# Optimization experiments

Hardware: AMD Instinct MI355X
Metric: run time of the kernel (lower is better)

## Reference

```python
import jax, jax.numpy as jnp
import numpy as np

USER = 100000
ITEM = 200000
N = USER + ITEM
LATDIM = 64
N_LAYERS = 3
N_EDGES = 9600000


def setup_inputs() -> dict:
    key = jax.random.key(0)
    k1, k2, k3, k4, k5 = jax.random.split(key, 5)
    # xavier_uniform for [N, latdim]: bound = sqrt(6/(fan_in+fan_out))
    bu = float(np.sqrt(6.0 / (USER + LATDIM)))
    bi = float(np.sqrt(6.0 / (ITEM + LATDIM)))
    uEmbeds = jax.random.uniform(k1, (USER, LATDIM), jnp.float32, -bu, bu)
    iEmbeds = jax.random.uniform(k2, (ITEM, LATDIM), jnp.float32, -bi, bi)
    edge_row = jax.random.randint(k3, (N_EDGES,), 0, N, dtype=jnp.int32)
    edge_col = jax.random.randint(k4, (N_EDGES,), 0, N, dtype=jnp.int32)
    edge_val = jax.random.uniform(k5, (N_EDGES,), jnp.float32) * 0.01
    return {"uEmbeds": uEmbeds, "iEmbeds": iEmbeds,
            "edge_row": edge_row, "edge_col": edge_col, "edge_val": edge_val}


def _spmm(row, col, val, x):
    # sparse adj (COO) @ dense x: gather cols, scale, scatter-add to rows
    msgs = x[col] * val[:, None]                 # [E, D]
    return jax.ops.segment_sum(msgs, row, num_segments=N)  # [N, D]


def reference(uEmbeds, iEmbeds, edge_row, edge_col, edge_val):
    # forward_gcn: multi-layer propagation, sum of all layer embeddings
    embeds = jnp.concatenate([uEmbeds, iEmbeds], axis=0)  # [N, D]
    acc = embeds
    cur = embeds
    for _ in range(N_LAYERS):
        cur = _spmm(edge_row, edge_col, edge_val, cur)
        acc = acc + cur
    return acc[:USER], acc[USER:]
```

## Files before the change

### kernel.cpp

```cpp
#include <hip/hip_runtime.h>
#include <hip/hip_bf16.h>

#define USER_N   100000
#define ITEM_N   200000
#define N_NODES  300000
#define LATDIM   64
#define N_EDGES  9600000
#define N_LAYERS 3

#define CSHIFT   11
#define CROWS    2048
#define NCOARSE  ((N_NODES + CROWS - 1) / CROWS)
#define CHUNK    4096
#define NCHUNKS  ((N_EDGES + CHUNK - 1) / CHUNK)
#define GPA      512

__device__ __forceinline__ unsigned short f2bf(float f) {
    unsigned int u = __float_as_uint(f);
    u += 0x7FFFu + ((u >> 16) & 1u);
    return (unsigned short)(u >> 16);
}
__device__ __forceinline__ float bf2f(unsigned short h) {
    return __uint_as_float(((unsigned int)h) << 16);
}

__global__ void cvt_concat_kernel(const float* __restrict__ u,
                                  const float* __restrict__ it,
                                  ushort4* __restrict__ cur0,
                                  int n4u, int n4total) {
    int stride = gridDim.x * blockDim.x;
    for (int i = blockIdx.x * blockDim.x + threadIdx.x; i < n4total; i += stride) {
        float4 v = (i < n4u) ? ((const float4*)u)[i]
                             : ((const float4*)it)[i - n4u];
        ushort4 o;
        o.x = f2bf(v.x); o.y = f2bf(v.y); o.z = f2bf(v.z); o.w = f2bf(v.w);
        cur0[i] = o;
    }
}

__global__ void h1_kernel(const int* __restrict__ row, int* __restrict__ ccnt) {
    __shared__ int h[NCOARSE];
    int t = threadIdx.x;
    if (t < NCOARSE) h[t] = 0;
    __syncthreads();
    int stride = gridDim.x * blockDim.x;
    for (int e = blockIdx.x * blockDim.x + t; e < N_EDGES; e += stride)
        atomicAdd(&h[row[e] >> CSHIFT], 1);
    __syncthreads();
    if (t < NCOARSE && h[t]) atomicAdd(&ccnt[t], h[t]);
}

__global__ void scan_coarse_kernel(const int* __restrict__ ccnt,
                                   int* __restrict__ cbase,
                                   int* __restrict__ cursorA,
                                   int* __restrict__ rowPtr) {
    __shared__ int lds[256];
    int t = threadIdx.x;
    int v = (t < NCOARSE) ? ccnt[t] : 0;
    lds[t] = v;
    __syncthreads();
    for (int off = 1; off < 256; off <<= 1) {
        int add = (t >= off) ? lds[t - off] : 0;
        __syncthreads();
        lds[t] += add;
        __syncthreads();
    }
    if (t < NCOARSE) { int ex = lds[t] - v; cbase[t] = ex; cursorA[t] = ex; }
    if (t == NCOARSE - 1) cbase[NCOARSE] = lds[t];
    if (t == 0) rowPtr[N_NODES] = N_EDGES;
}

__global__ __launch_bounds__(256)
void passA_kernel(const int*   __restrict__ row,
                  const int*   __restrict__ col,
                  const float* __restrict__ val,
                  int*         __restrict__ cursorA,
                  int2*        __restrict__ tempA) {
    __shared__ int2 stage[CHUNK];
    __shared__ unsigned char cb[CHUNK];
    __shared__ int h[NCOARSE];
    __shared__ int cur[NCOARSE];
    int t = threadIdx.x;
    for (int cid = blockIdx.x; cid < NCHUNKS; cid += gridDim.x) {
        if (t < NCOARSE) h[t] = 0;
        __syncthreads();
        int e0 = cid * CHUNK;
        int e1 = e0 + CHUNK; if (e1 > N_EDGES) e1 = N_EDGES;
        for (int e = e0 + t; e < e1; e += 256) {
            int r = row[e];
            int c = r >> CSHIFT;
            stage[e - e0] = make_int2(((r & (CROWS - 1)) << 19) | col[e],
                                      __float_as_int(val[e]));
            cb[e - e0] = (unsigned char)c;
            atomicAdd(&h[c], 1);
        }
        __syncthreads();
        if (t < NCOARSE) {
            int n = h[t];
            cur[t] = n ? atomicAdd(&cursorA[t], n) : 0;
        }
        __syncthreads();
        for (int e = e0 + t; e < e1; e += 256) {
            int c = cb[e - e0];
            int pos = atomicAdd(&cur[c], 1);
            tempA[pos] = stage[e - e0];
        }
        __syncthreads();
    }
}

__global__ __launch_bounds__(1024)
void passB_kernel(const int*  __restrict__ cbase,
                  const int2* __restrict__ tempA,
                  int2*       __restrict__ colval,
                  int*        __restrict__ rowPtr) {
    __shared__ int hist[CROWS];
    __shared__ int psum[1024];
    __shared__ int curs[CROWS];
    int c = blockIdx.x;
    int t = threadIdx.x;
    int beg = cbase[c], end = cbase[c + 1];

    hist[t] = 0; hist[t + 1024] = 0;
    __syncthreads();
    for (int i = beg + t; i < end; i += 1024)
        atomicAdd(&hist[((unsigned)tempA[i].x) >> 19], 1);
    __syncthreads();

    int b0 = hist[2 * t], b1 = hist[2 * t + 1];
    int tot = b0 + b1;
    psum[t] = tot;
    __syncthreads();
    for (int off = 1; off < 1024; off <<= 1) {
        int add = (t >= off) ? psum[t - off] : 0;
        __syncthreads();
        psum[t] += add;
        __syncthreads();
    }
    int ex = psum[t] - tot;
    int j0 = 2 * t, j1 = 2 * t + 1;
    int e0 = beg + ex, e1 = beg + ex + b0;
    curs[j0] = e0;
    curs[j1] = e1;
    int gr0 = c * CROWS + j0;
    int gr1 = c * CROWS + j1;
    if (gr0 < N_NODES) rowPtr[gr0] = e0;
    if (gr1 < N_NODES) rowPtr[gr1] = e1;
    __syncthreads();

    for (int i = beg + t; i < end; i += 1024) {
        int2 kv = tempA[i];
        int rl = ((unsigned)kv.x) >> 19;
        int pos = atomicAdd(&curs[rl], 1);
        colval[pos] = make_int2(kv.x & 0x7FFFF, kv.y);
    }
}

__global__ void spmm_bf16_kernel(const int*  __restrict__ rp,
                                 const int2* __restrict__ cv,
                                 const ushort4* __restrict__ x4,
                                 ushort4*       __restrict__ y4) {
    int g = (blockIdx.x * blockDim.x + threadIdx.x) >> 4;
    if (g >= N_NODES) return;
    int q = threadIdx.x & 15;
    int beg = rp[g];
    int end = rp[g + 1];

    float s0 = 0.f, s1 = 0.f, s2 = 0.f, s3 = 0.f;
    int i = beg;
    for (; i + 8 <= end; i += 8) {
        int2 cc[8]; ushort4 gg[8];
        #pragma unroll
        for (int k = 0; k < 8; ++k) cc[k] = cv[i + k];
        #pragma unroll
        for (int k = 0; k < 8; ++k) gg[k] = x4[(size_t)cc[k].x * 16 + q];
        #pragma unroll
        for (int k = 0; k < 8; ++k) {
            float v = __int_as_float(cc[k].y);
            s0 += bf2f(gg[k].x) * v; s1 += bf2f(gg[k].y) * v;
            s2 += bf2f(gg[k].z) * v; s3 += bf2f(gg[k].w) * v;
        }
    }
    for (; i < end; ++i) {
        int2 cc = cv[i];
        ushort4 gg = x4[(size_t)cc.x * 16 + q];
        float v = __int_as_float(cc.y);
        s0 += bf2f(gg.x) * v; s1 += bf2f(gg.y) * v;
        s2 += bf2f(gg.z) * v; s3 += bf2f(gg.w) * v;
    }

    ushort4 o;
    o.x = f2bf(s0); o.y = f2bf(s1); o.z = f2bf(s2); o.w = f2bf(s3);
    y4[(size_t)g * 16 + q] = o;
}

__global__ void final_acc_kernel(const float* __restrict__ u,
                                 const float* __restrict__ it,
                                 const ushort4* __restrict__ c1,
                                 const ushort4* __restrict__ c2,
                                 const ushort4* __restrict__ c3,
                                 float4* __restrict__ acc,
                                 int n4u, int n4total) {
    int stride = gridDim.x * blockDim.x;
    for (int i = blockIdx.x * blockDim.x + threadIdx.x; i < n4total; i += stride) {
        float4 e = (i < n4u) ? ((const float4*)u)[i]
                             : ((const float4*)it)[i - n4u];
        ushort4 a = c1[i], b = c2[i], c = c3[i];
        e.x += bf2f(a.x) + bf2f(b.x) + bf2f(c.x);
        e.y += bf2f(a.y) + bf2f(b.y) + bf2f(c.y);
        e.z += bf2f(a.z) + bf2f(b.z) + bf2f(c.z);
        e.w += bf2f(a.w) + bf2f(b.w) + bf2f(c.w);
        acc[i] = e;
    }
}

__global__ void copy_concat_kernel(const float* __restrict__ u,
                                   const float* __restrict__ it,
                                   float* __restrict__ cur,
                                   float* __restrict__ acc,
                                   int n4u, int n4total) {
    int stride = gridDim.x * blockDim.x;
    for (int i = blockIdx.x * blockDim.x + threadIdx.x; i < n4total; i += stride) {
        float4 v = (i < n4u) ? ((const float4*)u)[i]
                             : ((const float4*)it)[i - n4u];
        ((float4*)cur)[i] = v;
        ((float4*)acc)[i] = v;
    }
}

__global__ void spmm_atomic_kernel(const int*   __restrict__ row,
                                   const int*   __restrict__ col,
                                   const float* __restrict__ val,
                                   const float* __restrict__ x,
                                   float*       __restrict__ y) {
    const int total = N_EDGES * 16;
    int stride = gridDim.x * blockDim.x;
    for (int t = blockIdx.x * blockDim.x + threadIdx.x; t < total; t += stride) {
        int e = t >> 4;
        int q = t & 15;
        int r = row[e];
        int c = col[e];
        float v = val[e];
        float4 g = ((const float4*)x)[c * 16 + q];
        float* yp = y + r * 64 + q * 4;
        atomicAdd(yp + 0, g.x * v);
        atomicAdd(yp + 1, g.y * v);
        atomicAdd(yp + 2, g.z * v);
        atomicAdd(yp + 3, g.w * v);
    }
}

__global__ void acc_add_kernel(float* __restrict__ acc,
                               const float* __restrict__ add,
                               int n4) {
    int stride = gridDim.x * blockDim.x;
    for (int i = blockIdx.x * blockDim.x + threadIdx.x; i < n4; i += stride) {
        float4 a = ((const float4*)acc)[i];
        float4 b = ((const float4*)add)[i];
        a.x += b.x; a.y += b.y; a.z += b.z; a.w += b.w;
        ((float4*)acc)[i] = a;
    }
}

extern "C" void kernel_launch(void* const* d_in, const int* in_sizes, int n_in,
                              void* d_out, int out_size, void* d_ws, size_t ws_size,
                              hipStream_t stream) {
    const float* uEmb = (const float*)d_in[0];
    const float* iEmb = (const float*)d_in[1];
    const int*   row  = (const int*)  d_in[2];
    const int*   col  = (const int*)  d_in[3];
    const float* val  = (const float*)d_in[4];

    float* acc = (float*)d_out;

    const int n4total = N_NODES * (LATDIM / 4);
    const int n4u     = USER_N  * (LATDIM / 4);
    const size_t embBytes  = (size_t)N_NODES * LATDIM * sizeof(float);
    const size_t embBytesH = (size_t)N_NODES * LATDIM * 2;

    const int BLK = 256;
    const int GRID_MEM = 2048;

    auto align256 = [](size_t x) { return (x + 255) & ~(size_t)255; };
    size_t off = 0;
    size_t o_cur0   = off; off += align256(embBytesH);
    size_t o_c1     = off; off += align256(embBytesH);
    size_t o_c2     = off; off += align256(embBytesH);
    size_t o_c3     = off; off += align256(embBytesH);
    size_t o_colval = off; off += align256((size_t)N_EDGES * 8);
    size_t o_rowptr = off; off += align256(((size_t)N_NODES + 1) * 4);
    size_t o_ccnt   = off; off += align256((size_t)NCOARSE * 4);
    size_t o_cbase  = off; off += align256(((size_t)NCOARSE + 1) * 4);
    size_t o_cursA  = off; off += align256((size_t)NCOARSE * 4);
    size_t needed = off;

    char* wsb = (char*)d_ws;

    if (ws_size >= needed) {
        ushort4* cur0 = (ushort4*)(wsb + o_cur0);
        ushort4* c1   = (ushort4*)(wsb + o_c1);
        ushort4* c2   = (ushort4*)(wsb + o_c2);
        ushort4* c3   = (ushort4*)(wsb + o_c3);
        int2* colval  = (int2*)(wsb + o_colval);
        int2* tempA   = (int2*)(wsb + o_c1);
        int* rowPtr   = (int*)(wsb + o_rowptr);
        int* ccnt     = (int*)(wsb + o_ccnt);
        int* cbase    = (int*)(wsb + o_cbase);
        int* cursorA  = (int*)(wsb + o_cursA);

        cvt_concat_kernel<<<GRID_MEM, BLK, 0, stream>>>(uEmb, iEmb, cur0,
                                                        n4u, n4total);

        hipMemsetAsync(ccnt, 0, (size_t)NCOARSE * 4, stream);
        h1_kernel<<<GPA, 256, 0, stream>>>(row, ccnt);
        scan_coarse_kernel<<<1, 256, 0, stream>>>(ccnt, cbase, cursorA, rowPtr);
        passA_kernel<<<GPA, 256, 0, stream>>>(row, col, val, cursorA, tempA);
        passB_kernel<<<NCOARSE, 1024, 0, stream>>>(cbase, tempA, colval, rowPtr);

        const int GRID_SPMM = (N_NODES * 16 + BLK - 1) / BLK;
        spmm_bf16_kernel<<<GRID_SPMM, BLK, 0, stream>>>(rowPtr, colval, cur0, c1);
        spmm_bf16_kernel<<<GRID_SPMM, BLK, 0, stream>>>(rowPtr, colval, c1,   c2);
        spmm_bf16_kernel<<<GRID_SPMM, BLK, 0, stream>>>(rowPtr, colval, c2,   c3);

        final_acc_kernel<<<GRID_MEM, BLK, 0, stream>>>(uEmb, iEmb, c1, c2, c3,
                                                       (float4*)acc,
                                                       n4u, n4total);
    } else {
        float* cur = (float*)wsb;
        float* nxt = (float*)(wsb + embBytes);
        copy_concat_kernel<<<GRID_MEM, BLK, 0, stream>>>(uEmb, iEmb, cur, acc,
                                                         n4u, n4total);
        for (int l = 0; l < N_LAYERS; ++l) {
            hipMemsetAsync(nxt, 0, embBytes, stream);
            spmm_atomic_kernel<<<4096, BLK, 0, stream>>>(row, col, val, cur, nxt);
            acc_add_kernel<<<GRID_MEM, BLK, 0, stream>>>(acc, nxt, n4total);
            float* t = cur; cur = nxt; nxt = t;
        }
    }
}
```

Baseline: 878.3 us.

## Use finer coarse buckets, drop LDS staging in edge sort, prescale column indices

The coarse bucket width is halved and the chunk size doubled. passA no longer stages edges in LDS; it builds the histogram from one read of row and re-reads row, col and val when scattering, which frees shared memory for more resident blocks. passB now handles one row per thread with an in-place scan, and column indices are stored pre-multiplied by 16 so the SpMM gather drops the index multiply. The cost is an extra global read of row in passA and more coarse buckets to scan.

```diff
diff --git a/kernel.cpp b/kernel.cpp
--- a/kernel.cpp
+++ b/kernel.cpp
@@ -8,10 +8,10 @@
 #define N_EDGES  9600000
 #define N_LAYERS 3
 
-#define CSHIFT   11
-#define CROWS    2048
+#define CSHIFT   10
+#define CROWS    1024
 #define NCOARSE  ((N_NODES + CROWS - 1) / CROWS)
-#define CHUNK    4096
+#define CHUNK    8192
 #define NCHUNKS  ((N_EDGES + CHUNK - 1) / CHUNK)
 #define GPA      512
 
@@ -41,25 +41,26 @@
 __global__ void h1_kernel(const int* __restrict__ row, int* __restrict__ ccnt) {
     __shared__ int h[NCOARSE];
     int t = threadIdx.x;
-    if (t < NCOARSE) h[t] = 0;
+    for (int i = t; i < NCOARSE; i += 256) h[i] = 0;
     __syncthreads();
     int stride = gridDim.x * blockDim.x;
     for (int e = blockIdx.x * blockDim.x + t; e < N_EDGES; e += stride)
         atomicAdd(&h[row[e] >> CSHIFT], 1);
     __syncthreads();
-    if (t < NCOARSE && h[t]) atomicAdd(&ccnt[t], h[t]);
+    for (int i = t; i < NCOARSE; i += 256)
+        if (h[i]) atomicAdd(&ccnt[i], h[i]);
 }
 
 __global__ void scan_coarse_kernel(const int* __restrict__ ccnt,
                                    int* __restrict__ cbase,
                                    int* __restrict__ cursorA,
                                    int* __restrict__ rowPtr) {
-    __shared__ int lds[256];
+    __shared__ int lds[512];
     int t = threadIdx.x;
     int v = (t < NCOARSE) ? ccnt[t] : 0;
     lds[t] = v;
     __syncthreads();
-    for (int off = 1; off < 256; off <<= 1) {
+    for (int off = 1; off < 512; off <<= 1) {
         int add = (t >= off) ? lds[t - off] : 0;
         __syncthreads();
         lds[t] += add;
@@ -76,34 +77,28 @@
                   const float* __restrict__ val,
                   int*         __restrict__ cursorA,
                   int2*        __restrict__ tempA) {
-    __shared__ int2 stage[CHUNK];
-    __shared__ unsigned char cb[CHUNK];
     __shared__ int h[NCOARSE];
     __shared__ int cur[NCOARSE];
     int t = threadIdx.x;
     for (int cid = blockIdx.x; cid < NCHUNKS; cid += gridDim.x) {
-        if (t < NCOARSE) h[t] = 0;
+        for (int i = t; i < NCOARSE; i += 256) h[i] = 0;
         __syncthreads();
         int e0 = cid * CHUNK;
         int e1 = e0 + CHUNK; if (e1 > N_EDGES) e1 = N_EDGES;
+        for (int e = e0 + t; e < e1; e += 256)
+            atomicAdd(&h[row[e] >> CSHIFT], 1);
+        __syncthreads();
+        for (int i = t; i < NCOARSE; i += 256) {
+            int n = h[i];
+            cur[i] = n ? atomicAdd(&cursorA[i], n) : 0;
+        }
+        __syncthreads();
         for (int e = e0 + t; e < e1; e += 256) {
             int r = row[e];
             int c = r >> CSHIFT;
-            stage[e - e0] = make_int2(((r & (CROWS - 1)) << 19) | col[e],
-                                      __float_as_int(val[e]));
-            cb[e - e0] = (unsigned char)c;
-            atomicAdd(&h[c], 1);
-        }
-        __syncthreads();
-        if (t < NCOARSE) {
-            int n = h[t];
-            cur[t] = n ? atomicAdd(&cursorA[t], n) : 0;
-        }
-        __syncthreads();
-        for (int e = e0 + t; e < e1; e += 256) {
-            int c = cb[e - e0];
             int pos = atomicAdd(&cur[c], 1);
-            tempA[pos] = stage[e - e0];
+            tempA[pos] = make_int2(((r & (CROWS - 1)) << 19) | col[e],
+                                   __float_as_int(val[e]));
         }
         __syncthreads();
     }
@@ -115,44 +110,40 @@
                   int2*       __restrict__ colval,
                   int*        __restrict__ rowPtr) {
     __shared__ int hist[CROWS];
-    __shared__ int psum[1024];
     __shared__ int curs[CROWS];
     int c = blockIdx.x;
     int t = threadIdx.x;
     int beg = cbase[c], end = cbase[c + 1];
 
-    hist[t] = 0; hist[t + 1024] = 0;
+    hist[t] = 0;
     __syncthreads();
     for (int i = beg + t; i < end; i += 1024)
         atomicAdd(&hist[((unsigned)tempA[i].x) >> 19], 1);
     __syncthreads();
 
-    int b0 = hist[2 * t], b1 = hist[2 * t + 1];
-    int tot = b0 + b1;
-    psum[t] = tot;
+    int v = hist[t];
+    int inc = v;
+    __syncthreads();
+    hist[t] = inc;
     __syncthreads();
     for (int off = 1; off < 1024; off <<= 1) {
-        int add = (t >= off) ? psum[t - off] : 0;
-        __syncthreads();
-        psum[t] += add;
-        __syncthreads();
-    }
-    int ex = psum[t] - tot;
-    int j0 = 2 * t, j1 = 2 * t + 1;
-    int e0 = beg + ex, e1 = beg + ex + b0;
-    curs[j0] = e0;
-    curs[j1] = e1;
-    int gr0 = c * CROWS + j0;
-    int gr1 = c * CROWS + j1;
-    if (gr0 < N_NODES) rowPtr[gr0] = e0;
-    if (gr1 < N_NODES) rowPtr[gr1] = e1;
+        int add = (t >= off) ? hist[t - off] : 0;
+        __syncthreads();
+        hist[t] += add;
+        __syncthreads();
+    }
+    int ex = hist[t] - v;
+    int e0 = beg + ex;
+    curs[t] = e0;
+    int gr = c * CROWS + t;
+    if (gr < N_NODES) rowPtr[gr] = e0;
     __syncthreads();
 
     for (int i = beg + t; i < end; i += 1024) {
         int2 kv = tempA[i];
         int rl = ((unsigned)kv.x) >> 19;
         int pos = atomicAdd(&curs[rl], 1);
-        colval[pos] = make_int2(kv.x & 0x7FFFF, kv.y);
+        colval[pos] = make_int2((kv.x & 0x7FFFF) << 4, kv.y);
     }
 }
 
@@ -165,6 +156,7 @@
     int q = threadIdx.x & 15;
     int beg = rp[g];
     int end = rp[g + 1];
+    const ushort4* xq = x4 + q;
 
     float s0 = 0.f, s1 = 0.f, s2 = 0.f, s3 = 0.f;
     int i = beg;
@@ -173,7 +165,7 @@
         #pragma unroll
         for (int k = 0; k < 8; ++k) cc[k] = cv[i + k];
         #pragma unroll
-        for (int k = 0; k < 8; ++k) gg[k] = x4[(size_t)cc[k].x * 16 + q];
+        for (int k = 0; k < 8; ++k) gg[k] = xq[cc[k].x];
         #pragma unroll
         for (int k = 0; k < 8; ++k) {
             float v = __int_as_float(cc[k].y);
@@ -183,7 +175,7 @@
     }
     for (; i < end; ++i) {
         int2 cc = cv[i];
-        ushort4 gg = x4[(size_t)cc.x * 16 + q];
+        ushort4 gg = xq[cc.x];
         float v = __int_as_float(cc.y);
         s0 += bf2f(gg.x) * v; s1 += bf2f(gg.y) * v;
         s2 += bf2f(gg.z) * v; s3 += bf2f(gg.w) * v;
@@ -313,7 +305,7 @@
 
         hipMemsetAsync(ccnt, 0, (size_t)NCOARSE * 4, stream);
         h1_kernel<<<GPA, 256, 0, stream>>>(row, ccnt);
-        scan_coarse_kernel<<<1, 256, 0, stream>>>(ccnt, cbase, cursorA, rowPtr);
+        scan_coarse_kernel<<<1, 512, 0, stream>>>(ccnt, cbase, cursorA, rowPtr);
         passA_kernel<<<GPA, 256, 0, stream>>>(row, col, val, cursorA, tempA);
         passB_kernel<<<NCOARSE, 1024, 0, stream>>>(cbase, tempA, colval, rowPtr);
 
```

Result: slower. 953.4 us (+8.6%).

## Make coarse bucket scatter deterministic via per-chunk histogram scan and local sort

Applied to the files above, without the earlier changes.

Replaces the global-atomic cursor bucketing with a per-chunk histogram matrix, a per-bucket scan across chunks, and a coarse scan, so each chunk knows its exact output offsets. Inside each chunk, edges are locally sorted by bucket in shared memory, then written out contiguously to reduce scattered writes and global atomic contention. It also pre-shifts column indices by 16 so the SpMM gather skips an index multiply. The cost is an extra histogram pass over row, two scan kernels, and more workspace.

```diff
diff --git a/kernel.cpp b/kernel.cpp
--- a/kernel.cpp
+++ b/kernel.cpp
@@ -13,7 +13,8 @@
 #define NCOARSE  ((N_NODES + CROWS - 1) / CROWS)
 #define CHUNK    4096
 #define NCHUNKS  ((N_EDGES + CHUNK - 1) / CHUNK)
-#define GPA      512
+#define GP1      512
+#define GP4      768
 
 __device__ __forceinline__ unsigned short f2bf(float f) {
     unsigned int u = __float_as_uint(f);
@@ -38,25 +39,57 @@
     }
 }
 
-__global__ void h1_kernel(const int* __restrict__ row, int* __restrict__ ccnt) {
+__global__ __launch_bounds__(256)
+void p1_hist_kernel(const int* __restrict__ row, int* __restrict__ cntRaw) {
     __shared__ int h[NCOARSE];
     int t = threadIdx.x;
-    if (t < NCOARSE) h[t] = 0;
-    __syncthreads();
-    int stride = gridDim.x * blockDim.x;
-    for (int e = blockIdx.x * blockDim.x + t; e < N_EDGES; e += stride)
-        atomicAdd(&h[row[e] >> CSHIFT], 1);
-    __syncthreads();
-    if (t < NCOARSE && h[t]) atomicAdd(&ccnt[t], h[t]);
-}
-
-__global__ void scan_coarse_kernel(const int* __restrict__ ccnt,
-                                   int* __restrict__ cbase,
-                                   int* __restrict__ cursorA,
-                                   int* __restrict__ rowPtr) {
+    for (int k = blockIdx.x; k < NCHUNKS; k += gridDim.x) {
+        for (int i = t; i < NCOARSE; i += 256) h[i] = 0;
+        __syncthreads();
+        int e0 = k * CHUNK;
+        int e1 = e0 + CHUNK; if (e1 > N_EDGES) e1 = N_EDGES;
+        for (int e = e0 + t; e < e1; e += 256)
+            atomicAdd(&h[row[e] >> CSHIFT], 1);
+        __syncthreads();
+        for (int i = t; i < NCOARSE; i += 256)
+            cntRaw[i * NCHUNKS + k] = h[i];
+        __syncthreads();
+    }
+}
+
+__global__ __launch_bounds__(1024)
+void p2_scanchunks_kernel(const int* __restrict__ cntRaw,
+                          int* __restrict__ cntScan,
+                          int* __restrict__ btot) {
+    __shared__ int lds[1024];
+    int b = blockIdx.x, t = threadIdx.x;
+    const int base = t * 3;
+    int v0 = 0, v1 = 0, v2 = 0;
+    if (base     < NCHUNKS) v0 = cntRaw[b * NCHUNKS + base];
+    if (base + 1 < NCHUNKS) v1 = cntRaw[b * NCHUNKS + base + 1];
+    if (base + 2 < NCHUNKS) v2 = cntRaw[b * NCHUNKS + base + 2];
+    int s = v0 + v1 + v2;
+    lds[t] = s;
+    __syncthreads();
+    for (int off = 1; off < 1024; off <<= 1) {
+        int add = (t >= off) ? lds[t - off] : 0;
+        __syncthreads();
+        lds[t] += add;
+        __syncthreads();
+    }
+    int ex = lds[t] - s;
+    if (base     < NCHUNKS) cntScan[b * NCHUNKS + base]     = ex;
+    if (base + 1 < NCHUNKS) cntScan[b * NCHUNKS + base + 1] = ex + v0;
+    if (base + 2 < NCHUNKS) cntScan[b * NCHUNKS + base + 2] = ex + v0 + v1;
+    if (t == 1023) btot[b] = lds[1023];
+}
+
+__global__ void p3_scancoarse_kernel(const int* __restrict__ btot,
+                                     int* __restrict__ cbase,
+                                     int* __restrict__ rowPtr) {
     __shared__ int lds[256];
     int t = threadIdx.x;
-    int v = (t < NCOARSE) ? ccnt[t] : 0;
+    int v = (t < NCOARSE) ? btot[t] : 0;
     lds[t] = v;
     __syncthreads();
     for (int off = 1; off < 256; off <<= 1) {
@@ -65,46 +98,61 @@
         lds[t] += add;
         __syncthreads();
     }
-    if (t < NCOARSE) { int ex = lds[t] - v; cbase[t] = ex; cursorA[t] = ex; }
+    if (t < NCOARSE) cbase[t] = lds[t] - v;
     if (t == NCOARSE - 1) cbase[NCOARSE] = lds[t];
     if (t == 0) rowPtr[N_NODES] = N_EDGES;
 }
 
 __global__ __launch_bounds__(256)
-void passA_kernel(const int*   __restrict__ row,
-                  const int*   __restrict__ col,
-                  const float* __restrict__ val,
-                  int*         __restrict__ cursorA,
-                  int2*        __restrict__ tempA) {
+void p4_scatter_kernel(const int*   __restrict__ row,
+                       const int*   __restrict__ col,
+                       const float* __restrict__ val,
+                       const int*   __restrict__ cntRaw,
+                       const int*   __restrict__ cntScan,
+                       const int*   __restrict__ cbase,
+                       int2*        __restrict__ tempA) {
     __shared__ int2 stage[CHUNK];
-    __shared__ unsigned char cb[CHUNK];
-    __shared__ int h[NCOARSE];
-    __shared__ int cur[NCOARSE];
+    __shared__ int  dst[CHUNK];
+    __shared__ int  loff[NCOARSE];
+    __shared__ int  lcur[NCOARSE];
+    __shared__ int  gcur[NCOARSE];
+    __shared__ int  sc[256];
     int t = threadIdx.x;
-    for (int cid = blockIdx.x; cid < NCHUNKS; cid += gridDim.x) {
-        if (t < NCOARSE) h[t] = 0;
-        __syncthreads();
-        int e0 = cid * CHUNK;
+    for (int k = blockIdx.x; k < NCHUNKS; k += gridDim.x) {
+        int hv = 0;
+        if (t < NCOARSE) {
+            hv = cntRaw[t * NCHUNKS + k];
+            gcur[t] = cbase[t] + cntScan[t * NCHUNKS + k];
+        }
+        sc[t] = hv;
+        __syncthreads();
+        for (int off = 1; off < 256; off <<= 1) {
+            int add = (t >= off) ? sc[t - off] : 0;
+            __syncthreads();
+            sc[t] += add;
+            __syncthreads();
+        }
+        if (t < NCOARSE) {
+            int ex = sc[t] - hv;
+            loff[t] = ex;
+            lcur[t] = ex;
+        }
+        __syncthreads();
+
+        int e0 = k * CHUNK;
         int e1 = e0 + CHUNK; if (e1 > N_EDGES) e1 = N_EDGES;
+        int n = e1 - e0;
         for (int e = e0 + t; e < e1; e += 256) {
             int r = row[e];
             int c = r >> CSHIFT;
-            stage[e - e0] = make_int2(((r & (CROWS - 1)) << 19) | col[e],
-                                      __float_as_int(val[e]));
-            cb[e - e0] = (unsigned char)c;
-            atomicAdd(&h[c], 1);
-        }
-        __syncthreads();
-        if (t < NCOARSE) {
-            int n = h[t];
-            cur[t] = n ? atomicAdd(&cursorA[t], n) : 0;
-        }
-        __syncthreads();
-        for (int e = e0 + t; e < e1; e += 256) {
-            int c = cb[e - e0];
-            int pos = atomicAdd(&cur[c], 1);
-            tempA[pos] = stage[e - e0];
-        }
+            int p = atomicAdd(&lcur[c], 1);
+            stage[p] = make_int2(((r & (CROWS - 1)) << 19) | col[e],
+                                 __float_as_int(val[e]));
+            dst[p] = gcur[c] + (p - loff[c]);
+        }
+        __syncthreads();
+        for (int j = t; j < n; j += 256)
+            tempA[dst[j]] = stage[j];
         __syncthreads();
     }
 }
@@ -152,7 +200,7 @@
         int2 kv = tempA[i];
         int rl = ((unsigned)kv.x) >> 19;
         int pos = atomicAdd(&curs[rl], 1);
-        colval[pos] = make_int2(kv.x & 0x7FFFF, kv.y);
+        colval[pos] = make_int2((kv.x & 0x7FFFF) << 4, kv.y);
     }
 }
 
@@ -165,6 +213,7 @@
     int q = threadIdx.x & 15;
     int beg = rp[g];
     int end = rp[g + 1];
+    const ushort4* xq = x4 + q;
 
     float s0 = 0.f, s1 = 0.f, s2 = 0.f, s3 = 0.f;
     int i = beg;
@@ -173,7 +222,7 @@
         #pragma unroll
         for (int k = 0; k < 8; ++k) cc[k] = cv[i + k];
         #pragma unroll
-        for (int k = 0; k < 8; ++k) gg[k] = x4[(size_t)cc[k].x * 16 + q];
+        for (int k = 0; k < 8; ++k) gg[k] = xq[cc[k].x];
         #pragma unroll
         for (int k = 0; k < 8; ++k) {
             float v = __int_as_float(cc[k].y);
@@ -183,7 +232,7 @@
     }
     for (; i < end; ++i) {
         int2 cc = cv[i];
-        ushort4 gg = x4[(size_t)cc.x * 16 + q];
+        ushort4 gg = xq[cc.x];
         float v = __int_as_float(cc.y);
         s0 += bf2f(gg.x) * v; s1 += bf2f(gg.y) * v;
         s2 += bf2f(gg.z) * v; s3 += bf2f(gg.w) * v;
@@ -289,9 +338,10 @@
     size_t o_c3     = off; off += align256(embBytesH);
     size_t o_colval = off; off += align256((size_t)N_EDGES * 8);
     size_t o_rowptr = off; off += align256(((size_t)N_NODES + 1) * 4);
-    size_t o_ccnt   = off; off += align256((size_t)NCOARSE * 4);
+    size_t o_craw   = off; off += align256((size_t)NCOARSE * NCHUNKS * 4);
+    size_t o_cscan  = off; off += align256((size_t)NCOARSE * NCHUNKS * 4);
+    size_t o_btot   = off; off += align256((size_t)NCOARSE * 4);
     size_t o_cbase  = off; off += align256(((size_t)NCOARSE + 1) * 4);
-    size_t o_cursA  = off; off += align256((size_t)NCOARSE * 4);
     size_t needed = off;
 
     char* wsb = (char*)d_ws;
@@ -304,18 +354,21 @@
         int2* colval  = (int2*)(wsb + o_colval);
         int2* tempA   = (int2*)(wsb + o_c1);
         int* rowPtr   = (int*)(wsb + o_rowptr);
-        int* ccnt     = (int*)(wsb + o_ccnt);
+        int* cntRaw   = (int*)(wsb + o_craw);
+        int* cntScan  = (int*)(wsb + o_cscan);
+        int* btot     = (int*)(wsb + o_btot);
         int* cbase    = (int*)(wsb + o_cbase);
-        int* cursorA  = (int*)(wsb + o_cursA);
 
         cvt_concat_kernel<<<GRID_MEM, BLK, 0, stream>>>(uEmb, iEmb, cur0,
                                                         n4u, n4total);
 
-        hipMemsetAsync(ccnt, 0, (size_t)NCOARSE * 4, stream);
-        h1_kernel<<<GPA, 256, 0, stream>>>(row, ccnt);
-        scan_coarse_kernel<<<1, 256, 0, stream>>>(ccnt, cbase, cursorA, rowPtr);
-        passA_kernel<<<GPA, 256, 0, stream>>>(row, col, val, cursorA, tempA);
-        passB_kernel<<<NCOARSE, 1024, 0, stream>>>(cbase, tempA, colval, rowPtr);
+        p1_hist_kernel      <<<GP1, 256, 0, stream>>>(row, cntRaw);
+        p2_scanchunks_kernel<<<NCOARSE, 1024, 0, stream>>>(cntRaw, cntScan, btot);
+        p3_scancoarse_kernel<<<1, 256, 0, stream>>>(btot, cbase, rowPtr);
+        p4_scatter_kernel   <<<GP4, 256, 0, stream>>>(row, col, val, cntRaw,
+                                                      cntScan, cbase, tempA);
+        passB_kernel        <<<NCOARSE, 1024, 0, stream>>>(cbase, tempA,
+                                                           colval, rowPtr);
 
         const int GRID_SPMM = (N_NODES * 16 + BLK - 1) / BLK;
         spmm_bf16_kernel<<<GRID_SPMM, BLK, 0, stream>>>(rowPtr, colval, cur0, c1);
```

After: 854.7 us. -2.7%, faster.
